# Kernel tuning notes

Hardware: AMD Instinct MI355X
Metric: run time of the kernel (lower is better)

The kernel has to match this reference:

```python
import jax, jax.numpy as jnp
import numpy as np

B, N, H = 2, 4096, 2048
NH, HD = 16, 128
BLK = 256
EPS = 1e-6


def setup_inputs() -> dict:
    key = jax.random.key(0)
    ks = jax.random.split(key, 5)
    scale = 0.02
    x = jax.random.normal(ks[0], (B, N, H), dtype=jnp.float32)
    # ALiBi-style per-head slopes, shape [h,1,1]
    slopes = (1.0 / (2.0 ** (8.0 * np.arange(1, NH + 1) / NH))).astype(np.float32)
    slope_rate = jnp.asarray(slopes).reshape(NH, 1, 1)
    w_qkv = jax.random.normal(ks[1], (3 * NH * HD, H), dtype=jnp.float32) * scale
    w_gate = jax.random.normal(ks[2], (NH * HD, H), dtype=jnp.float32) * scale
    w_out = jax.random.normal(ks[3], (H, NH * HD), dtype=jnp.float32) * scale
    norm_w = jnp.ones((NH * HD,), dtype=jnp.float32)
    return {"hidden_states": x, "slope_rate": slope_rate, "w_qkv": w_qkv,
            "w_gate": w_gate, "w_out": w_out, "norm_w": norm_w}


def _lightning_attn(x, slope_rate, w_qkv, w_gate, w_out, norm_w):
    b, n, _ = x.shape
    h, d = NH, HD
    nb = n // BLK
    # qkv projection + activation
    qkv = jax.nn.silu(jnp.einsum('bnf,of->bno', x, w_qkv))        # [b,n,3hd]
    qkv = qkv.reshape(b, n, h, 3 * d)
    q, k, v = jnp.split(qkv, 3, axis=-1)                          # each [b,n,h,d]
    q = q.transpose(0, 2, 1, 3)                                   # [b,h,n,d]
    k = k.transpose(0, 2, 1, 3)
    v = v.transpose(0, 2, 1, 3)

    s = slope_rate.astype(jnp.float32)                            # [h,1,1]
    arr = jnp.arange(1, BLK + 1, dtype=jnp.float32)               # 1..BLOCK
    q_decay = jnp.exp(-s * arr[:, None])                          # [h,BLK,1]
    k_decay = jnp.exp(-s * (BLK - arr)[:, None])                  # [h,BLK,1]
    idx = arr[:, None] - arr[None, :]                             # [BLK,BLK]
    diag_decay = jnp.where(idx >= 0, jnp.exp(-s * idx), 0.0)      # [h,BLK,BLK]
    block_decay = jnp.exp(-s * BLK)                               # [h,1,1]

    # split sequence into blocks; scan axis leading
    qb = q.reshape(b, h, nb, BLK, d).transpose(2, 0, 1, 3, 4)     # [nb,b,h,BLK,d]
    kb = k.reshape(b, h, nb, BLK, d).transpose(2, 0, 1, 3, 4)
    vb = v.reshape(b, h, nb, BLK, d).transpose(2, 0, 1, 3, 4)

    def step(kv, blk):
        qi, ki, vi = blk                                          # [b,h,BLK,d]
        o_inter = jnp.einsum('bhmd,bhde->bhme', qi * q_decay, kv)
        qk = jnp.einsum('bhmd,bhnd->bhmn', qi, ki) * diag_decay
        o_intra = jnp.einsum('bhmn,bhne->bhme', qk, vi)
        kv_new = block_decay * kv + jnp.einsum('bhmd,bhme->bhde', ki * k_decay, vi)
        return kv_new, o_inter + o_intra

    kv0 = jnp.zeros((b, h, d, d), dtype=jnp.float32)
    _, out = jax.lax.scan(step, kv0, (qb, kb, vb))                # [nb,b,h,BLK,d]
    out = out.transpose(1, 2, 0, 3, 4).reshape(b, h, n, d)        # [b,h,n,d]
    out = out.transpose(0, 2, 1, 3).reshape(b, n, h * d)          # [b,n,h*d]

    # RMSNorm (fp32)
    var = jnp.mean(out * out, axis=-1, keepdims=True)
    out = norm_w * (out * jax.lax.rsqrt(var + EPS))

    gate = jax.nn.sigmoid(jnp.einsum('bnf,of->bno', x, w_gate))
    return jnp.einsum('bno,fo->bnf', gate * out, w_out)


def reference(hidden_states, slope_rate, w_qkv, w_gate, w_out, norm_w):
    return _lightning_attn(hidden_states, slope_rate, w_qkv, w_gate, w_out, norm_w)
```

## Files before the change

### kernel.cpp

```cpp
#include <hip/hip_runtime.h>
#include <hip/hip_bf16.h>
#include <stdint.h>


typedef __bf16 bf16_t;
typedef __bf16 bf16x8 __attribute__((ext_vector_type(8)));
typedef __bf16 bf16x4 __attribute__((ext_vector_type(4)));
typedef float  f32x4  __attribute__((ext_vector_type(4)));

#define AS1C(p) ((const __attribute__((address_space(1))) void*)(p))
#define AS3(p)  ((__attribute__((address_space(3))) void*)(p))

__global__ __launch_bounds__(256)
void cvt4_kernel(const float* __restrict__ s0, bf16_t* __restrict__ d0, int n0,
                 const float* __restrict__ s1, bf16_t* __restrict__ d1, int n1,
                 const float* __restrict__ s2, bf16_t* __restrict__ d2, int n2,
                 const float* __restrict__ s3, bf16_t* __restrict__ d3, int n3) {
    const int total = n0 + n1 + n2 + n3;
    const int stride = gridDim.x * blockDim.x;
    for (int i = blockIdx.x * blockDim.x + threadIdx.x; i < total; i += stride) {
        const float* s; bf16_t* d; int j = i;
        if (j < n0) { s = s0; d = d0; }
        else {
            j -= n0;
            if (j < n1) { s = s1; d = d1; }
            else {
                j -= n1;
                if (j < n2) { s = s2; d = d2; }
                else { j -= n2; s = s3; d = d3; }
            }
        }
        float4 v = ((const float4*)s)[j];
        bf16x4 o;
        o[0] = (bf16_t)v.x; o[1] = (bf16_t)v.y; o[2] = (bf16_t)v.z; o[3] = (bf16_t)v.w;
        ((bf16x4*)d)[j] = o;
    }
}

template <int EPI>
__global__ __launch_bounds__(512)
void gemm6(const bf16_t* __restrict__ A, const bf16_t* __restrict__ Bm,
           int M, int N, int K,
           float* __restrict__ outf, bf16_t* __restrict__ outb,
           bf16_t* __restrict__ qb, bf16_t* __restrict__ kb,
           bf16_t* __restrict__ kT, bf16_t* __restrict__ vT,
           const float* __restrict__ slopes) {
    __shared__ char lds[2][65536];
    const int tid = threadIdx.x, w = tid >> 6, lane = tid & 63;
    const int l15 = lane & 15, lq = lane >> 4;
    const int wr = w >> 2, wc = w & 3;

    const int nwg = gridDim.x;
    const int cpx = nwg >> 3;
    const int id = blockIdx.x;
    const int sw = (id & 7) * cpx + (id >> 3);
    const int gx = N >> 8;
    const int tm = (sw / gx) << 8;
    const int tn = (sw % gx) << 8;
    const int nt = K >> 6;

    auto stageA1 = [&](char* dst, int t1, int j) {
        const bf16_t* base = A + (size_t)tm * K + t1 * 64;
        const int c = tid + j * 512;
        const int r = c >> 3, sl = c & 7;
        __builtin_amdgcn_global_load_lds(
            AS1C(base + (size_t)r * K + ((sl ^ (r & 7)) << 3)),
            AS3(dst + c * 16), 16, 0, 0);
    };
    auto stageB1 = [&](char* dst, int t1, int j) {
        const bf16_t* base = Bm + (size_t)tn * K + t1 * 64;
        const int c = tid + j * 512;
        const int r = c >> 3, sl = c & 7;
        __builtin_amdgcn_global_load_lds(
            AS1C(base + (size_t)r * K + ((sl ^ (r & 7)) << 3)),
            AS3(dst + 32768 + c * 16), 16, 0, 0);
    };

    f32x4 acc[8][4] = {};

    {
        char* d0 = &lds[0][0];
        stageA1(d0, 0, 0); stageA1(d0, 0, 1); stageA1(d0, 0, 2); stageA1(d0, 0, 3);
        stageB1(d0, 0, 0); stageB1(d0, 0, 1); stageB1(d0, 0, 2); stageB1(d0, 0, 3);
    }

    for (int t = 0; t < nt; ++t) {
        const char* cur = &lds[t & 1][0];
        char* nxt = &lds[1 - (t & 1)][0];
        const bool pre = (t + 1 < nt);

        asm volatile("s_waitcnt vmcnt(0)" ::: "memory");
        __builtin_amdgcn_s_barrier();
        __builtin_amdgcn_sched_barrier(0);

        bf16x8 bfr[4][2], af[4][2];
#pragma unroll
        for (int n = 0; n < 4; ++n)
#pragma unroll
            for (int kk = 0; kk < 2; ++kk) {
                const int row = wc * 64 + n * 16 + l15;
                bfr[n][kk] = *(const bf16x8*)(cur + 32768 + row * 128 + ((((kk << 2) | lq) ^ (row & 7)) << 4));
            }
#pragma unroll
        for (int m = 0; m < 4; ++m)
#pragma unroll
            for (int kk = 0; kk < 2; ++kk) {
                const int row = wr * 128 + m * 16 + l15;
                af[m][kk] = *(const bf16x8*)(cur + row * 128 + ((((kk << 2) | lq) ^ (row & 7)) << 4));
            }
        if (pre) {
            stageA1(nxt, t + 1, 0); stageA1(nxt, t + 1, 1);
            stageA1(nxt, t + 1, 2); stageA1(nxt, t + 1, 3);
            stageB1(nxt, t + 1, 0); stageB1(nxt, t + 1, 1);
            stageB1(nxt, t + 1, 2); stageB1(nxt, t + 1, 3);
        }
        __builtin_amdgcn_s_setprio(1);
#pragma unroll
        for (int m = 0; m < 4; ++m)
#pragma unroll
            for (int n = 0; n < 4; ++n)
#pragma unroll
                for (int kk = 0; kk < 2; ++kk)
                    acc[m][n] = __builtin_amdgcn_mfma_f32_16x16x32_bf16(af[m][kk], bfr[n][kk], acc[m][n], 0, 0, 0);
        __builtin_amdgcn_s_setprio(0);

#pragma unroll
        for (int m = 0; m < 4; ++m)
#pragma unroll
            for (int kk = 0; kk < 2; ++kk) {
                const int row = wr * 128 + 64 + m * 16 + l15;
                af[m][kk] = *(const bf16x8*)(cur + row * 128 + ((((kk << 2) | lq) ^ (row & 7)) << 4));
            }
        __builtin_amdgcn_s_setprio(1);
#pragma unroll
        for (int m = 0; m < 4; ++m)
#pragma unroll
            for (int n = 0; n < 4; ++n)
#pragma unroll
                for (int kk = 0; kk < 2; ++kk)
                    acc[4 + m][n] = __builtin_amdgcn_mfma_f32_16x16x32_bf16(af[m][kk], bfr[n][kk], acc[4 + m][n], 0, 0, 0);
        __builtin_amdgcn_s_setprio(0);
    }

#pragma unroll
    for (int m = 0; m < 8; ++m) {
#pragma unroll
        for (int n = 0; n < 4; ++n) {
            const int colb = tn + wc * 64 + n * 16;
            if (EPI == 2) {
#pragma unroll
                for (int r = 0; r < 4; ++r) {
                    const int row = tm + wr * 128 + m * 16 + lq * 4 + r;
                    outf[(size_t)row * N + colb + l15] = acc[m][n][r];
                }
            } else if (EPI == 1) {
#pragma unroll
                for (int r = 0; r < 4; ++r) {
                    const int row = tm + wr * 128 + m * 16 + lq * 4 + r;
                    const float v = acc[m][n][r];
                    outb[(size_t)row * N + colb + l15] = (bf16_t)(1.f / (1.f + __expf(-v)));
                }
            } else {
                const int head = colb / 384;
                const int jj = colb % 384;
                const int row0 = tm + wr * 128 + m * 16 + lq * 4;
                const int bidx = row0 >> 12;
                const int nn0 = row0 & 4095;
                const size_t bh = (size_t)(bidx * 16 + head);
                float sv[4];
#pragma unroll
                for (int r = 0; r < 4; ++r) {
                    const float v = acc[m][n][r];
                    sv[r] = v / (1.f + __expf(-v));
                }
                if (jj < 128) {
                    bf16_t* qp = qb + (bh * 4096 + nn0) * 128 + jj + l15;
#pragma unroll
                    for (int r = 0; r < 4; ++r) qp[(size_t)r * 128] = (bf16_t)sv[r];
                } else if (jj < 256) {
                    bf16_t* kp = kb + (bh * 4096 + nn0) * 128 + (jj - 128) + l15;
#pragma unroll
                    for (int r = 0; r < 4; ++r) kp[(size_t)r * 128] = (bf16_t)sv[r];
                    bf16x4 pk;
#pragma unroll
                    for (int r = 0; r < 4; ++r) pk[r] = (bf16_t)sv[r];
                    *(bf16x4*)(kT + bh * 524288 + (size_t)(jj - 128 + l15) * 4096 + nn0) = pk;
                } else {
                    bf16x4 pv;
#pragma unroll
                    for (int r = 0; r < 4; ++r) pv[r] = (bf16_t)sv[r];
                    *(bf16x4*)(vT + bh * 524288 + (size_t)(jj - 256 + l15) * 4096 + nn0) = pv;
                }
            }
        }
    }
}

__global__ __launch_bounds__(256)
void pass_ct(const bf16_t* __restrict__ vT, const bf16_t* __restrict__ kT,
             float* __restrict__ CT, const float* __restrict__ slopes) {
    const int idx = blockIdx.x, bh = idx >> 4, j = idx & 15;
    const float s = slopes[bh & 15];
    const float r_ = __expf(s);
    const int tid = threadIdx.x, w = tid >> 6, lane = tid & 63;
    const int l15 = lane & 15, lq = lane >> 4;
    const int we = (w & 1) * 64, wd = (w >> 1) * 64;
    const bf16_t* va = vT + (size_t)bh * 524288 + j * 256;
    const bf16_t* ka = kT + (size_t)bh * 524288 + j * 256;
    f32x4 acc[4][4] = {};
#pragma unroll
    for (int kk = 0; kk < 8; ++kk) {
        float fdec[8];
        fdec[0] = __expf(-s * (float)(255 - (kk * 32 + lq * 8)));
#pragma unroll
        for (int t = 1; t < 8; ++t) fdec[t] = fdec[t - 1] * r_;
        bf16x8 af[4], bfv[4];
#pragma unroll
        for (int et = 0; et < 4; ++et)
            af[et] = *(const bf16x8*)(va + (size_t)(we + et * 16 + l15) * 4096 + kk * 32 + lq * 8);
#pragma unroll
        for (int dt = 0; dt < 4; ++dt) {
            bf16x8 raw = *(const bf16x8*)(ka + (size_t)(wd + dt * 16 + l15) * 4096 + kk * 32 + lq * 8);
#pragma unroll
            for (int t = 0; t < 8; ++t) bfv[dt][t] = (bf16_t)((float)raw[t] * fdec[t]);
        }
#pragma unroll
        for (int et = 0; et < 4; ++et)
#pragma unroll
            for (int dt = 0; dt < 4; ++dt)
                acc[et][dt] = __builtin_amdgcn_mfma_f32_16x16x32_bf16(af[et], bfv[dt], acc[et][dt], 0, 0, 0);
    }
    float* out = CT + (size_t)idx * 16384;
#pragma unroll
    for (int et = 0; et < 4; ++et)
#pragma unroll
        for (int dt = 0; dt < 4; ++dt)
#pragma unroll
            for (int r = 0; r < 4; ++r)
                out[(size_t)(we + et * 16 + lq * 4 + r) * 128 + wd + dt * 16 + l15] = acc[et][dt][r];
}

__global__ __launch_bounds__(256)
void scan_kv(const float* __restrict__ CT, bf16_t* __restrict__ states,
             const float* __restrict__ slopes) {
    const int gid = blockIdx.x * 256 + threadIdx.x;
    const int bh = gid >> 14, elem = gid & 16383;
    const float s = slopes[bh & 15];
    const float bd = __expf(-s * 256.f);
    const float* c = CT + (size_t)bh * 16 * 16384 + elem;
    bf16_t* st = states + (size_t)bh * 16 * 16384 + elem;
    float kv = 0.f;
#pragma unroll
    for (int j = 0; j < 16; ++j) {
        st[(size_t)j * 16384] = (bf16_t)kv;
        kv = bd * kv + c[(size_t)j * 16384];
    }
}

__global__ __launch_bounds__(512)
void pass_attn(const bf16_t* __restrict__ qb, const bf16_t* __restrict__ kb,
               const bf16_t* __restrict__ vT, const bf16_t* __restrict__ states,
               const float* __restrict__ slopes, bf16_t* __restrict__ outattn) {
    __shared__ bf16_t scratch[8][16][40];
    const int idx = blockIdx.x, bh = idx >> 4, j = idx & 15;
    const int b = bh >> 4, h = bh & 15;
    const int tid = threadIdx.x, w = tid >> 6, lane = tid & 63;
    const int l15 = lane & 15, lq = lane >> 4;
    const float s = slopes[h];
    f32x4 o[2][8] = {};
    float rowf[4];
#pragma unroll
    for (int r = 0; r < 4; ++r) rowf[r] = __expf(-s * (float)(lq * 4 + r));

    const size_t qrow = (size_t)bh * 4096 + j * 256;
    const bf16_t* qbase = qb + qrow * 128;
    const bf16_t* kbp = kb + qrow * 128;
    const bf16_t* vtp = vT + (size_t)bh * 524288 + (size_t)j * 256;

#pragma unroll
    for (int gi = 0; gi < 2; ++gi) {
        const int gg = gi ? (15 - w) : w;
        const bf16_t* qg = qbase + (size_t)(gg * 16) * 128;
        bf16x8 qf[4];
#pragma unroll
        for (int kq = 0; kq < 4; ++kq)
            qf[kq] = *(const bf16x8*)(qg + (size_t)l15 * 128 + kq * 32 + lq * 8);
        const int ncmax = gg >> 1;
        for (int nc = 0; nc <= ncmax; ++nc) {
            f32x4 sacc[2] = {};
#pragma unroll
            for (int kq = 0; kq < 4; ++kq) {
                bf16x8 b0 = *(const bf16x8*)(kbp + (size_t)(nc * 32 + l15) * 128 + kq * 32 + lq * 8);
                bf16x8 b1 = *(const bf16x8*)(kbp + (size_t)(nc * 32 + 16 + l15) * 128 + kq * 32 + lq * 8);
                sacc[0] = __builtin_amdgcn_mfma_f32_16x16x32_bf16(qf[kq], b0, sacc[0], 0, 0, 0);
                sacc[1] = __builtin_amdgcn_mfma_f32_16x16x32_bf16(qf[kq], b1, sacc[1], 0, 0, 0);
            }
#pragma unroll
            for (int nt = 0; nt < 2; ++nt) {
                const float colf = __expf(s * (float)(nc * 32 + nt * 16 + l15 - gg * 16));
#pragma unroll
                for (int r = 0; r < 4; ++r) {
                    const int mloc = lq * 4 + r;
                    const int nglob = nc * 32 + nt * 16 + l15;
                    const float f = (gg * 16 + mloc >= nglob) ? rowf[r] * colf : 0.f;
                    scratch[w][mloc][nt * 16 + l15] = (bf16_t)(sacc[nt][r] * f);
                }
            }
            bf16x8 sa = *(const bf16x8*)&scratch[w][l15][lq * 8];
            __builtin_amdgcn_s_setprio(1);
#pragma unroll
            for (int et = 0; et < 8; ++et) {
                bf16x8 bv = *(const bf16x8*)(vtp + (size_t)(et * 16 + l15) * 4096 + nc * 32 + lq * 8);
                o[gi][et] = __builtin_amdgcn_mfma_f32_16x16x32_bf16(sa, bv, o[gi][et], 0, 0, 0);
            }
            __builtin_amdgcn_s_setprio(0);
        }
    }

    float rq[2];
    rq[0] = __expf(-s * (float)(w * 16 + l15 + 1));
    rq[1] = __expf(-s * (float)((15 - w) * 16 + l15 + 1));
    const bf16_t* st = states + (size_t)idx * 16384;
#pragma unroll
    for (int kq = 0; kq < 4; ++kq) {
        bf16x8 aq[2];
#pragma unroll
        for (int gi = 0; gi < 2; ++gi) {
            const int gg = gi ? (15 - w) : w;
            bf16x8 raw = *(const bf16x8*)(qbase + (size_t)(gg * 16 + l15) * 128 + kq * 32 + lq * 8);
#pragma unroll
            for (int t = 0; t < 8; ++t) aq[gi][t] = (bf16_t)((float)raw[t] * rq[gi]);
        }
        __builtin_amdgcn_s_setprio(1);
#pragma unroll
        for (int et = 0; et < 8; ++et) {
            bf16x8 bs = *(const bf16x8*)(st + (size_t)(et * 16 + l15) * 128 + kq * 32 + lq * 8);
            o[0][et] = __builtin_amdgcn_mfma_f32_16x16x32_bf16(aq[0], bs, o[0][et], 0, 0, 0);
            o[1][et] = __builtin_amdgcn_mfma_f32_16x16x32_bf16(aq[1], bs, o[1][et], 0, 0, 0);
        }
        __builtin_amdgcn_s_setprio(0);
    }

    bf16_t* opb = outattn + ((size_t)b * 4096 + j * 256) * 2048 + h * 128;
#pragma unroll
    for (int gi = 0; gi < 2; ++gi) {
        const int gg = gi ? (15 - w) : w;
#pragma unroll
        for (int et = 0; et < 8; ++et)
#pragma unroll
            for (int r = 0; r < 4; ++r)
                opb[(size_t)(gg * 16 + lq * 4 + r) * 2048 + et * 16 + l15] = (bf16_t)o[gi][et][r];
    }
}

__global__ __launch_bounds__(256)
void rmsnorm_gate(const bf16_t* __restrict__ attn, const bf16_t* __restrict__ gate_s,
                  const float* __restrict__ norm_w, bf16_t* __restrict__ gout) {
    const int row = blockIdx.x, tid = threadIdx.x;
    const bf16x8 a8 = *(const bf16x8*)(attn + (size_t)row * 2048 + tid * 8);
    float av[8];
#pragma unroll
    for (int i = 0; i < 8; ++i) av[i] = (float)a8[i];
    float ss = 0.f;
#pragma unroll
    for (int i = 0; i < 8; ++i) ss += av[i] * av[i];
#pragma unroll
    for (int off = 32; off; off >>= 1) ss += __shfl_xor(ss, off);
    __shared__ float red[4];
    if ((tid & 63) == 0) red[tid >> 6] = ss;
    __syncthreads();
    const float rr = rsqrtf((red[0] + red[1] + red[2] + red[3]) * (1.0f / 2048.f) + 1e-6f);
    const bf16x8 g = *(const bf16x8*)(gate_s + (size_t)row * 2048 + tid * 8);
    const float* nw = norm_w + tid * 8;
    bf16x8 res;
#pragma unroll
    for (int i = 0; i < 8; ++i) res[i] = (bf16_t)((float)g[i] * nw[i] * av[i] * rr);
    *(bf16x8*)(gout + (size_t)row * 2048 + tid * 8) = res;
}

extern "C" void kernel_launch(void* const* d_in, const int* in_sizes, int n_in,
                              void* d_out, int out_size, void* d_ws, size_t ws_size,
                              hipStream_t stream) {
    (void)in_sizes; (void)n_in; (void)out_size;
    const float* x      = (const float*)d_in[0];
    const float* slopes = (const float*)d_in[1];
    const float* w_qkv  = (const float*)d_in[2];
    const float* w_gate = (const float*)d_in[3];
    const float* w_out  = (const float*)d_in[4];
    const float* norm_w = (const float*)d_in[5];
    float* out = (float*)d_out;
    char* ws = (char*)d_ws;

    size_t off = 0;
    auto alloc = [&](size_t bytes) { char* p = ws + off; off += (bytes + 255) & ~(size_t)255; return p; };
    bf16_t* xb     = (bf16_t*)alloc(8192ull * 2048 * 2);
    bf16_t* wqkvb  = (bf16_t*)alloc(6144ull * 2048 * 2);
    bf16_t* wgateb = (bf16_t*)alloc(2048ull * 2048 * 2);
    bf16_t* woutb  = (bf16_t*)alloc(2048ull * 2048 * 2);
    bf16_t* qb     = (bf16_t*)alloc(33554432);
    bf16_t* kb     = (bf16_t*)alloc(33554432);
    char*   ctbuf  = alloc(33554432);
    bf16_t* vT     = (bf16_t*)alloc(33554432);
    bf16_t* kT     = (bf16_t*)alloc(33554432);
    if (ws_size < off) return;
    float*  CT     = (float*)ctbuf;
    bf16_t* gate_s = kT;
    bf16_t* states = (bf16_t*)wqkvb;
    bf16_t* attn_s = (bf16_t*)out;
    bf16_t* gout   = qb;

    cvt4_kernel<<<2048, 256, 0, stream>>>(
        x,      xb,     8192 * 2048 / 4,
        w_qkv,  wqkvb,  6144 * 2048 / 4,
        w_gate, wgateb, 2048 * 2048 / 4,
        w_out,  woutb,  2048 * 2048 / 4);
    gemm6<0><<<768, 512, 0, stream>>>(xb, wqkvb, 8192, 6144, 2048,
        nullptr, nullptr, qb, kb, kT, vT, slopes);
    pass_ct<<<512, 256, 0, stream>>>(vT, kT, CT, slopes);
    gemm6<1><<<256, 512, 0, stream>>>(xb, wgateb, 8192, 2048, 2048,
        nullptr, gate_s, nullptr, nullptr, nullptr, nullptr, nullptr);
    scan_kv<<<2048, 256, 0, stream>>>(CT, states, slopes);
    pass_attn<<<512, 512, 0, stream>>>(qb, kb, vT, states, slopes, attn_s);
    rmsnorm_gate<<<8192, 256, 0, stream>>>(attn_s, gate_s, norm_w, gout);
    gemm6<2><<<256, 512, 0, stream>>>(gout, woutb, 8192, 2048, 2048,
        out, nullptr, nullptr, nullptr, nullptr, nullptr, nullptr);
}
```

Before: 492.2 us.

## Add finer-grained pipelined QKV GEMM kernel interleaving prefetch with MFMA phases

Adds a dedicated gemm8 kernel for the QKV projection that splits each K-tile into four MFMA phases. Next-tile global-to-LDS loads are issued in chunks between those phases, with partial vmcnt waits in place of a full drain at the top of each iteration. The goal is to overlap global memory traffic with matrix math in the largest GEMM. In exchange it adds more barriers per iteration and reloads A fragments in smaller pieces. The other GEMMs keep the old schedule, with the unused epilogue parameters removed.

```diff
diff --git a/kernel.cpp b/kernel.cpp
--- a/kernel.cpp
+++ b/kernel.cpp
@@ -37,14 +37,11 @@
     }
 }
 
-template <int EPI>
 __global__ __launch_bounds__(512)
-void gemm6(const bf16_t* __restrict__ A, const bf16_t* __restrict__ Bm,
+void gemm8(const bf16_t* __restrict__ A, const bf16_t* __restrict__ Bm,
            int M, int N, int K,
-           float* __restrict__ outf, bf16_t* __restrict__ outb,
            bf16_t* __restrict__ qb, bf16_t* __restrict__ kb,
-           bf16_t* __restrict__ kT, bf16_t* __restrict__ vT,
-           const float* __restrict__ slopes) {
+           bf16_t* __restrict__ kT, bf16_t* __restrict__ vT) {
     __shared__ char lds[2][65536];
     const int tid = threadIdx.x, w = tid >> 6, lane = tid & 63;
     const int l15 = lane & 15, lq = lane >> 4;
@@ -80,6 +77,182 @@
 
     {
         char* d0 = &lds[0][0];
+        stageB1(d0, 0, 0); stageB1(d0, 0, 1); stageB1(d0, 0, 2); stageB1(d0, 0, 3);
+        stageA1(d0, 0, 0); stageA1(d0, 0, 2);
+        stageA1(d0, 0, 1); stageA1(d0, 0, 3);
+    }
+    asm volatile("s_waitcnt vmcnt(2)" ::: "memory");
+    __builtin_amdgcn_s_barrier();
+    __builtin_amdgcn_sched_barrier(0);
+
+    for (int t = 0; t < nt; ++t) {
+        const char* cur = &lds[t & 1][0];
+        char* nxt = &lds[1 - (t & 1)][0];
+        const bool pre = (t + 1 < nt);
+        bf16x8 bfr[4][2], af[4];
+
+#pragma unroll
+        for (int n = 0; n < 4; ++n)
+#pragma unroll
+            for (int kk = 0; kk < 2; ++kk) {
+                const int row = wc * 64 + n * 16 + l15;
+                bfr[n][kk] = *(const bf16x8*)(cur + 32768 + row * 128 + ((((kk << 2) | lq) ^ (row & 7)) << 4));
+            }
+#pragma unroll
+        for (int m = 0; m < 4; ++m) {
+            const int row = wr * 128 + m * 16 + l15;
+            af[m] = *(const bf16x8*)(cur + row * 128 + ((lq ^ (row & 7)) << 4));
+        }
+        if (pre) { stageB1(nxt, t + 1, 0); stageB1(nxt, t + 1, 1); stageB1(nxt, t + 1, 2); }
+        __builtin_amdgcn_s_barrier();
+        asm volatile("s_waitcnt lgkmcnt(0)" ::: "memory");
+        __builtin_amdgcn_sched_barrier(0);
+        __builtin_amdgcn_s_setprio(1);
+#pragma unroll
+        for (int m = 0; m < 4; ++m)
+#pragma unroll
+            for (int n = 0; n < 4; ++n)
+                acc[m][n] = __builtin_amdgcn_mfma_f32_16x16x32_bf16(af[m], bfr[n][0], acc[m][n], 0, 0, 0);
+        __builtin_amdgcn_s_setprio(0);
+        __builtin_amdgcn_s_barrier();
+
+#pragma unroll
+        for (int m = 0; m < 4; ++m) {
+            const int row = wr * 128 + m * 16 + l15;
+            af[m] = *(const bf16x8*)(cur + row * 128 + (((4 | lq) ^ (row & 7)) << 4));
+        }
+        if (pre) { stageB1(nxt, t + 1, 3); stageA1(nxt, t + 1, 0); stageA1(nxt, t + 1, 2); }
+        __builtin_amdgcn_s_barrier();
+        asm volatile("s_waitcnt lgkmcnt(0)" ::: "memory");
+        __builtin_amdgcn_sched_barrier(0);
+        __builtin_amdgcn_s_setprio(1);
+#pragma unroll
+        for (int m = 0; m < 4; ++m)
+#pragma unroll
+            for (int n = 0; n < 4; ++n)
+                acc[m][n] = __builtin_amdgcn_mfma_f32_16x16x32_bf16(af[m], bfr[n][1], acc[m][n], 0, 0, 0);
+        __builtin_amdgcn_s_setprio(0);
+        if (pre) asm volatile("s_waitcnt vmcnt(6)" ::: "memory");
+        else     asm volatile("s_waitcnt vmcnt(0)" ::: "memory");
+        __builtin_amdgcn_s_barrier();
+
+#pragma unroll
+        for (int m = 0; m < 4; ++m) {
+            const int row = wr * 128 + 64 + m * 16 + l15;
+            af[m] = *(const bf16x8*)(cur + row * 128 + ((lq ^ (row & 7)) << 4));
+        }
+        if (pre) { stageA1(nxt, t + 1, 1); stageA1(nxt, t + 1, 3); }
+        __builtin_amdgcn_s_barrier();
+        asm volatile("s_waitcnt lgkmcnt(0)" ::: "memory");
+        __builtin_amdgcn_sched_barrier(0);
+        __builtin_amdgcn_s_setprio(1);
+#pragma unroll
+        for (int m = 0; m < 4; ++m)
+#pragma unroll
+            for (int n = 0; n < 4; ++n)
+                acc[4 + m][n] = __builtin_amdgcn_mfma_f32_16x16x32_bf16(af[m], bfr[n][0], acc[4 + m][n], 0, 0, 0);
+        __builtin_amdgcn_s_setprio(0);
+        __builtin_amdgcn_s_barrier();
+
+#pragma unroll
+        for (int m = 0; m < 4; ++m) {
+            const int row = wr * 128 + 64 + m * 16 + l15;
+            af[m] = *(const bf16x8*)(cur + row * 128 + (((4 | lq) ^ (row & 7)) << 4));
+        }
+        __builtin_amdgcn_s_barrier();
+        asm volatile("s_waitcnt lgkmcnt(0)" ::: "memory");
+        __builtin_amdgcn_sched_barrier(0);
+        __builtin_amdgcn_s_setprio(1);
+#pragma unroll
+        for (int m = 0; m < 4; ++m)
+#pragma unroll
+            for (int n = 0; n < 4; ++n)
+                acc[4 + m][n] = __builtin_amdgcn_mfma_f32_16x16x32_bf16(af[m], bfr[n][1], acc[4 + m][n], 0, 0, 0);
+        __builtin_amdgcn_s_setprio(0);
+        if (pre) asm volatile("s_waitcnt vmcnt(2)" ::: "memory");
+        __builtin_amdgcn_s_barrier();
+        __builtin_amdgcn_sched_barrier(0);
+    }
+
+#pragma unroll
+    for (int m = 0; m < 8; ++m) {
+#pragma unroll
+        for (int n = 0; n < 4; ++n) {
+            const int colb = tn + wc * 64 + n * 16;
+            const int head = colb / 384;
+            const int jj = colb % 384;
+            const int row0 = tm + wr * 128 + m * 16 + lq * 4;
+            const int bidx = row0 >> 12;
+            const int nn0 = row0 & 4095;
+            const size_t bh = (size_t)(bidx * 16 + head);
+            float sv[4];
+#pragma unroll
+            for (int r = 0; r < 4; ++r) {
+                const float v = acc[m][n][r];
+                sv[r] = v / (1.f + __expf(-v));
+            }
+            if (jj < 128) {
+                bf16_t* qp = qb + (bh * 4096 + nn0) * 128 + jj + l15;
+#pragma unroll
+                for (int r = 0; r < 4; ++r) qp[(size_t)r * 128] = (bf16_t)sv[r];
+            } else if (jj < 256) {
+                bf16_t* kp = kb + (bh * 4096 + nn0) * 128 + (jj - 128) + l15;
+#pragma unroll
+                for (int r = 0; r < 4; ++r) kp[(size_t)r * 128] = (bf16_t)sv[r];
+                bf16x4 pk;
+#pragma unroll
+                for (int r = 0; r < 4; ++r) pk[r] = (bf16_t)sv[r];
+                *(bf16x4*)(kT + bh * 524288 + (size_t)(jj - 128 + l15) * 4096 + nn0) = pk;
+            } else {
+                bf16x4 pv;
+#pragma unroll
+                for (int r = 0; r < 4; ++r) pv[r] = (bf16_t)sv[r];
+                *(bf16x4*)(vT + bh * 524288 + (size_t)(jj - 256 + l15) * 4096 + nn0) = pv;
+            }
+        }
+    }
+}
+
+template <int EPI>
+__global__ __launch_bounds__(512)
+void gemm6(const bf16_t* __restrict__ A, const bf16_t* __restrict__ Bm,
+           int M, int N, int K,
+           float* __restrict__ outf, bf16_t* __restrict__ outb) {
+    __shared__ char lds[2][65536];
+    const int tid = threadIdx.x, w = tid >> 6, lane = tid & 63;
+    const int l15 = lane & 15, lq = lane >> 4;
+    const int wr = w >> 2, wc = w & 3;
+
+    const int nwg = gridDim.x;
+    const int cpx = nwg >> 3;
+    const int id = blockIdx.x;
+    const int sw = (id & 7) * cpx + (id >> 3);
+    const int gx = N >> 8;
+    const int tm = (sw / gx) << 8;
+    const int tn = (sw % gx) << 8;
+    const int nt = K >> 6;
+
+    auto stageA1 = [&](char* dst, int t1, int j) {
+        const bf16_t* base = A + (size_t)tm * K + t1 * 64;
+        const int c = tid + j * 512;
+        const int r = c >> 3, sl = c & 7;
+        __builtin_amdgcn_global_load_lds(
+            AS1C(base + (size_t)r * K + ((sl ^ (r & 7)) << 3)),
+            AS3(dst + c * 16), 16, 0, 0);
+    };
+    auto stageB1 = [&](char* dst, int t1, int j) {
+        const bf16_t* base = Bm + (size_t)tn * K + t1 * 64;
+        const int c = tid + j * 512;
+        const int r = c >> 3, sl = c & 7;
+        __builtin_amdgcn_global_load_lds(
+            AS1C(base + (size_t)r * K + ((sl ^ (r & 7)) << 3)),
+            AS3(dst + 32768 + c * 16), 16, 0, 0);
+    };
+
+    f32x4 acc[8][4] = {};
+
+    {
+        char* d0 = &lds[0][0];
         stageA1(d0, 0, 0); stageA1(d0, 0, 1); stageA1(d0, 0, 2); stageA1(d0, 0, 3);
         stageB1(d0, 0, 0); stageB1(d0, 0, 1); stageB1(d0, 0, 2); stageB1(d0, 0, 3);
     }
@@ -153,43 +326,12 @@
                     const int row = tm + wr * 128 + m * 16 + lq * 4 + r;
                     outf[(size_t)row * N + colb + l15] = acc[m][n][r];
                 }
-            } else if (EPI == 1) {
+            } else {
 #pragma unroll
                 for (int r = 0; r < 4; ++r) {
                     const int row = tm + wr * 128 + m * 16 + lq * 4 + r;
                     const float v = acc[m][n][r];
                     outb[(size_t)row * N + colb + l15] = (bf16_t)(1.f / (1.f + __expf(-v)));
-                }
-            } else {
-                const int head = colb / 384;
-                const int jj = colb % 384;
-                const int row0 = tm + wr * 128 + m * 16 + lq * 4;
-                const int bidx = row0 >> 12;
-                const int nn0 = row0 & 4095;
-                const size_t bh = (size_t)(bidx * 16 + head);
-                float sv[4];
-#pragma unroll
-                for (int r = 0; r < 4; ++r) {
-                    const float v = acc[m][n][r];
-                    sv[r] = v / (1.f + __expf(-v));
-                }
-                if (jj < 128) {
-                    bf16_t* qp = qb + (bh * 4096 + nn0) * 128 + jj + l15;
-#pragma unroll
-                    for (int r = 0; r < 4; ++r) qp[(size_t)r * 128] = (bf16_t)sv[r];
-                } else if (jj < 256) {
-                    bf16_t* kp = kb + (bh * 4096 + nn0) * 128 + (jj - 128) + l15;
-#pragma unroll
-                    for (int r = 0; r < 4; ++r) kp[(size_t)r * 128] = (bf16_t)sv[r];
-                    bf16x4 pk;
-#pragma unroll
-                    for (int r = 0; r < 4; ++r) pk[r] = (bf16_t)sv[r];
-                    *(bf16x4*)(kT + bh * 524288 + (size_t)(jj - 128 + l15) * 4096 + nn0) = pk;
-                } else {
-                    bf16x4 pv;
-#pragma unroll
-                    for (int r = 0; r < 4; ++r) pv[r] = (bf16_t)sv[r];
-                    *(bf16x4*)(vT + bh * 524288 + (size_t)(jj - 256 + l15) * 4096 + nn0) = pv;
                 }
             }
         }
@@ -414,14 +556,14 @@
         w_qkv,  wqkvb,  6144 * 2048 / 4,
         w_gate, wgateb, 2048 * 2048 / 4,
         w_out,  woutb,  2048 * 2048 / 4);
-    gemm6<0><<<768, 512, 0, stream>>>(xb, wqkvb, 8192, 6144, 2048,
-        nullptr, nullptr, qb, kb, kT, vT, slopes);
+    gemm8<<<768, 512, 0, stream>>>(xb, wqkvb, 8192, 6144, 2048,
+        qb, kb, kT, vT);
     pass_ct<<<512, 256, 0, stream>>>(vT, kT, CT, slopes);
     gemm6<1><<<256, 512, 0, stream>>>(xb, wgateb, 8192, 2048, 2048,
-        nullptr, gate_s, nullptr, nullptr, nullptr, nullptr, nullptr);
+        nullptr, gate_s);
     scan_kv<<<2048, 256, 0, stream>>>(CT, states, slopes);
     pass_attn<<<512, 512, 0, stream>>>(qb, kb, vT, states, slopes, attn_s);
     rmsnorm_gate<<<8192, 256, 0, stream>>>(attn_s, gate_s, norm_w, gout);
     gemm6<2><<<256, 512, 0, stream>>>(gout, woutb, 8192, 2048, 2048,
-        out, nullptr, nullptr, nullptr, nullptr, nullptr, nullptr);
-}
+        out, nullptr);
+}
```

After: 505.6 us. 1.03x slower.
